# Performance work log

Measured on AMD Instinct MI355X. Metric: run time of the kernel, lower is better.

## Reference

```python
import jax, jax.numpy as jnp
import numpy as np

B, S, E, H, D, F = 8, 512, 768, 12, 64, 3072
EPS = 1e-5
SQRT3 = np.float32(np.sqrt(3.0))


def _ln(x, g, b):
    m = jnp.mean(x, -1, keepdims=True)
    v = jnp.mean((x - m) ** 2, -1, keepdims=True)
    return (x - m) * jax.lax.rsqrt(v + EPS) * g + b


def _gelu_new(x):
    return 0.5 * x * (1.0 + jnp.tanh(0.7978845608028654 * (x + 0.044715 * x * x * x)))


def _heads(t):  # [B,T,E] -> [B,T,H,D]
    return t.reshape(t.shape[0], t.shape[1], H, D)


def _self_attn(xl, Wq, Wk, Wv, Wo, bo, mask):
    q = _heads(xl @ Wq)
    k = _heads(xl @ Wk)
    v = _heads(xl @ Wv)
    w = jnp.einsum('bqhd,bkhd->bhqk', q, k) / 8.0  # scale=True, sqrt(64)
    w = jnp.where(mask, -1e9, w)
    p = jax.nn.softmax(w, axis=-1)
    o = jnp.einsum('bhqk,bkhd->bqhd', p, v).reshape(xl.shape)
    present = jnp.stack([k.transpose(0, 2, 1, 3), v.transpose(0, 2, 1, 3)])  # [2,B,H,S,D]
    return o @ Wo + bo, present


def _cross_attn(xl, el, wq, bq, wk, bk, wv, bv, wp, bp, mask):
    q = _heads(xl @ wq + bq)
    k = _heads(el @ wk + bk)
    v = _heads(el @ wv + bv)
    w = jnp.einsum('bqhd,bkhd->bhqk', q, k) / 8.0
    w = jnp.where(mask, -1e4, w)
    p = jax.nn.softmax(w, axis=-1)
    o = jnp.einsum('bhqk,bkhd->bqhd', p, v).reshape(xl.shape)
    return o @ wp + bp  # Conv1D: x @ W + b


def _block(x, encoder_output, mask_queries, mask_sa, mask_enc, tau,
           Wq, Wk, Wv, Wo, bo,
           fcq_w, fcq_b, fck_w, fck_b, fcv_w, fcv_b, cproj_w, cproj_b,
           ln1_g, ln1_b, ln2_g, ln2_b,
           cfc_w, cfc_b, cproj2_w, cproj2_b,
           a1_w, a1_b, a2_w, a2_b, a3_w, a3_b):
    thr = jnp.asarray(tau, jnp.float32)
    sa, present = _self_attn(_ln(x, ln1_g, ln1_b), Wq, Wk, Wv, Wo, bo, mask_sa)
    a = x + sa  # resid dropout = identity (eval)
    al = _ln(a, ln1_g, ln1_b)

    def cross(idx):
        el = _ln(encoder_output[:, idx], ln1_g, ln1_b)
        return _cross_attn(al, el, fcq_w, fcq_b, fck_w, fck_b, fcv_w, fcv_b,
                           cproj_w, cproj_b, mask_enc)

    e1, e2, e3 = cross(0), cross(1), cross(2)

    def gate(e, w, b):
        alpha = jax.nn.sigmoid(jnp.concatenate([a, e], -1) @ w + b)
        lm = jnp.where(alpha > thr, 1.0, 0.0)
        vm = jnp.where(alpha < 1.0 - thr, 1.0, 0.0)
        return alpha * lm * a + (1.0 - alpha) * vm * e

    enc_att = (gate(e1, a1_w, a1_b) + gate(e2, a2_w, a2_b) + gate(e3, a3_w, a3_b)) / SQRT3
    aq = enc_att * mask_queries
    m = _gelu_new(_ln(aq, ln2_g, ln2_b) @ cfc_w + cfc_b) @ cproj2_w + cproj2_b
    out = (aq + m) * mask_queries
    return out, present


def setup_inputs() -> dict:
    key = jax.random.key(0)
    ks = jax.random.split(key, 40)
    p = lambda k, shp: (jax.random.normal(k, shp, jnp.float32) * 0.02)
    x = jax.random.normal(ks[0], (B, S, E), jnp.float32)
    encoder_output = jax.random.normal(ks[1], (B, 3, S, E), jnp.float32)
    mask_queries = jnp.ones((B, S, 1), jnp.float32)
    causal = ~jnp.tril(jnp.ones((S, S), bool))  # True = masked
    mask_self_attention = jnp.broadcast_to(causal[None, None], (B, 1, S, S))
    mask_encoder = jax.random.bernoulli(ks[2], 0.1, (B, 1, 1, S))
    d = dict(x=x, encoder_output=encoder_output, mask_queries=mask_queries,
             mask_self_attention=mask_self_attention, mask_encoder=mask_encoder,
             i=0, tau=0,
             Wq=p(ks[3], (E, E)), Wk=p(ks[4], (E, E)), Wv=p(ks[5], (E, E)),
             Wo=p(ks[6], (E, E)), bo=jnp.zeros((E,), jnp.float32),
             fcq_w=p(ks[7], (E, E)), fcq_b=jnp.zeros((E,), jnp.float32),
             fck_w=p(ks[8], (E, E)), fck_b=jnp.zeros((E,), jnp.float32),
             fcv_w=p(ks[9], (E, E)), fcv_b=jnp.zeros((E,), jnp.float32),
             cproj_w=p(ks[10], (E, E)), cproj_b=jnp.zeros((E,), jnp.float32),
             ln1_g=jnp.ones((E,), jnp.float32), ln1_b=jnp.zeros((E,), jnp.float32),
             ln2_g=jnp.ones((E,), jnp.float32), ln2_b=jnp.zeros((E,), jnp.float32),
             cfc_w=p(ks[11], (E, F)), cfc_b=jnp.zeros((F,), jnp.float32),
             cproj2_w=p(ks[12], (F, E)), cproj2_b=jnp.zeros((E,), jnp.float32),
             a1_w=p(ks[13], (2 * E, E)), a1_b=jnp.zeros((E,), jnp.float32),
             a2_w=p(ks[14], (2 * E, E)), a2_b=jnp.zeros((E,), jnp.float32),
             a3_w=p(ks[15], (2 * E, E)), a3_b=jnp.zeros((E,), jnp.float32))
    return d


def reference(x, encoder_output, mask_queries, mask_self_attention, mask_encoder, i, tau,
              Wq, Wk, Wv, Wo, bo,
              fcq_w, fcq_b, fck_w, fck_b, fcv_w, fcv_b, cproj_w, cproj_b,
              ln1_g, ln1_b, ln2_g, ln2_b,
              cfc_w, cfc_b, cproj2_w, cproj2_b,
              a1_w, a1_b, a2_w, a2_b, a3_w, a3_b):
    return _block(x, encoder_output, mask_queries, mask_self_attention, mask_encoder, tau,
                  Wq, Wk, Wv, Wo, bo,
                  fcq_w, fcq_b, fck_w, fck_b, fcv_w, fcv_b, cproj_w, cproj_b,
                  ln1_g, ln1_b, ln2_g, ln2_b,
                  cfc_w, cfc_b, cproj2_w, cproj2_b,
                  a1_w, a1_b, a2_w, a2_b, a3_w, a3_b)
```

## Files before the change

kernel.cpp:

```cpp
#include <hip/hip_runtime.h>
#include <hip/hip_bf16.h>
#include <math.h>

typedef __hip_bfloat16 bf16;
typedef __attribute__((ext_vector_type(8))) short s16x8;
typedef __attribute__((ext_vector_type(4))) float f32x4;

#define BB 8
#define SS 512
#define EE 768
#define HH 12
#define DD 64
#define FF 3072
#define NTOK (BB * SS)
#define NE ((size_t)NTOK * EE)

#define TM 128
#define TN 128
#define TK 64

#define QT 64
#define KT 64

#define FLAG_RES  4
#define FLAG_GELU 8
#define FLAG_FIN  16
#define FLAG_CBSD 32
#define FLAG_QKV  128
#define FLAG_KV   256
#define FLAG_GSEG 512

#define AS1 const __attribute__((address_space(1))) void*
#define AS3 __attribute__((address_space(3))) void*

__device__ __forceinline__ float gelu_new(float x) {
    float u2 = 1.5957691216057308f * (x + 0.044715f * x * x * x);
    return x / (1.0f + __expf(-u2));
}

__global__ __launch_bounds__(256) void tcast_kernel(
    const float* __restrict__ src, bf16* __restrict__ dst, int R, int C)
{
    __shared__ float t[32][33];
    int c0 = blockIdx.x * 32, r0 = blockIdx.y * 32;
    int tid = threadIdx.x;
    int x = tid & 31, y = tid >> 5;
    #pragma unroll
    for (int i = 0; i < 4; ++i) {
        int r = y + i * 8;
        t[r][x] = src[(size_t)(r0 + r) * C + c0 + x];
    }
    __syncthreads();
    #pragma unroll
    for (int i = 0; i < 4; ++i) {
        int c = y + i * 8;
        dst[(size_t)(c0 + c) * R + r0 + x] = __float2bfloat16(t[x][c]);
    }
}

__global__ __launch_bounds__(256) void ln_kernel(
    const float* __restrict__ in, bf16* __restrict__ out,
    const float* __restrict__ g, const float* __restrict__ bta, int encmode)
{
    int row = blockIdx.x;
    const float* x;
    if (encmode) {
        int idx = row >> 12, b = (row >> 9) & 7, s = row & 511;
        x = in + (((size_t)b * 3 + idx) * SS + s) * EE;
    } else {
        x = in + (size_t)row * EE;
    }
    int tid = threadIdx.x;

    float v0 = x[tid], v1 = x[tid + 256], v2 = x[tid + 512];
    float s1 = v0 + v1 + v2;
    float s2 = v0 * v0 + v1 * v1 + v2 * v2;
    #pragma unroll
    for (int o = 32; o > 0; o >>= 1) {
        s1 += __shfl_down(s1, o);
        s2 += __shfl_down(s2, o);
    }
    __shared__ float r1[4], r2[4];
    if ((tid & 63) == 0) { r1[tid >> 6] = s1; r2[tid >> 6] = s2; }
    __syncthreads();
    float mean = (r1[0] + r1[1] + r1[2] + r1[3]) * (1.0f / 768.0f);
    float ssq  = (r2[0] + r2[1] + r2[2] + r2[3]) * (1.0f / 768.0f);
    float rstd = rsqrtf(ssq - mean * mean + 1e-5f);

    bf16* y = out + (size_t)row * EE;
    y[tid]       = __float2bfloat16((v0 - mean) * rstd * g[tid]       + bta[tid]);
    y[tid + 256] = __float2bfloat16((v1 - mean) * rstd * g[tid + 256] + bta[tid + 256]);
    y[tid + 512] = __float2bfloat16((v2 - mean) * rstd * g[tid + 512] + bta[tid + 512]);
}

template <int FLAGS>
__global__ __launch_bounds__(256) void mgemm_kernel(
    const bf16* __restrict__ A, const bf16* __restrict__ A2,
    const bf16* __restrict__ Wt, const float* __restrict__ bias,
    float* __restrict__ Cf, bf16* __restrict__ Cb, bf16* __restrict__ Cb2,
    int ldcb, const float* __restrict__ Rsrc, const float* __restrict__ maskq,
    int Nn, int K, int lda)
{
    constexpr bool f_res  = FLAGS & FLAG_RES;
    constexpr bool f_gelu = FLAGS & FLAG_GELU;
    constexpr bool f_fin  = FLAGS & FLAG_FIN;
    constexpr bool f_cbsd = FLAGS & FLAG_CBSD;
    constexpr bool f_qkv  = FLAGS & FLAG_QKV;
    constexpr bool f_kv   = FLAGS & FLAG_KV;
    constexpr bool f_gseg = FLAGS & FLAG_GSEG;

    __shared__ __align__(16) bf16 smem[2 * (TM * TK + TN * TK)];
    const int BUFE = TM * TK + TN * TK;
    int tid = threadIdx.x;
    int w = tid >> 6, l = tid & 63;
    int row0 = blockIdx.x * TM, col0 = blockIdx.y * TN;

    int wr = (w >> 1) * 64, wc = (w & 1) * 64;
    int lr = l & 15, lg = l >> 4;

    const bf16* Wb = Wt;
    const float* bb_ = bias;
    if constexpr (f_gseg) {
        int seg = row0 >> 12;
        Wb = Wt + (size_t)seg * 1536 * 768;
        bb_ = bias + seg * 768;
    }

    f32x4 acc[4][4];
    #pragma unroll
    for (int m = 0; m < 4; ++m)
        #pragma unroll
        for (int n = 0; n < 4; ++n) acc[m][n] = (f32x4){0.f, 0.f, 0.f, 0.f};

    auto stage = [&](int buf, int kb) {
        bf16* As_ = smem + buf * BUFE;
        bf16* Bs_ = As_ + TM * TK;
        #pragma unroll
        for (int i = 0; i < 4; ++i) {
            int e = (i * 256 + tid) * 8;
            int r = e >> 6;
            int c = (e & 63) ^ ((r & 7) << 3);
            const bf16* asrc;
            if constexpr (f_gseg) {
                int kg = kb + c;
                if (kg < 768) asrc = A  + (size_t)((row0 + r) & 4095) * lda + kg;
                else          asrc = A2 + (size_t)(row0 + r) * lda + (kg - 768);
            } else {
                asrc = A + (size_t)(row0 + r) * lda + kb + c;
            }
            __builtin_amdgcn_global_load_lds((AS1)asrc,
                (AS3)((char*)As_ + i * 4096 + w * 1024), 16, 0, 0);
            __builtin_amdgcn_global_load_lds((AS1)(Wb + (size_t)(col0 + r) * K + kb + c),
                (AS3)((char*)Bs_ + i * 4096 + w * 1024), 16, 0, 0);
        }
    };

    int nk = K / TK;
    stage(0, 0);
    for (int t = 0; t < nk; ++t) {
        int cur = t & 1;
        if (t + 1 < nk) {
            stage(cur ^ 1, (t + 1) * TK);
            asm volatile("s_waitcnt vmcnt(8)" ::: "memory");
        } else {
            asm volatile("s_waitcnt vmcnt(0)" ::: "memory");
        }
        __builtin_amdgcn_s_barrier();
        __builtin_amdgcn_sched_barrier(0);

        const char* As = (const char*)(smem + cur * BUFE);
        const char* Bs = As + TM * TK * 2;
        __builtin_amdgcn_s_setprio(1);
        #pragma unroll
        for (int ks = 0; ks < 2; ++ks) {
            s16x8 af[4], bfr[4];
            #pragma unroll
            for (int m = 0; m < 4; ++m) {
                int row = wr + m * 16 + lr;
                af[m] = *(const s16x8*)(As + row * 128 +
                          ((ks * 64 + lg * 16) ^ ((row & 7) << 4)));
            }
            #pragma unroll
            for (int n = 0; n < 4; ++n) {
                int row = wc + n * 16 + lr;
                bfr[n] = *(const s16x8*)(Bs + row * 128 +
                          ((ks * 64 + lg * 16) ^ ((row & 7) << 4)));
            }
            #pragma unroll
            for (int m = 0; m < 4; ++m)
                #pragma unroll
                for (int n = 0; n < 4; ++n)
                    acc[m][n] = __builtin_amdgcn_mfma_f32_16x16x32_bf16(
                        af[m], bfr[n], acc[m][n], 0, 0, 0);
        }
        __builtin_amdgcn_s_setprio(0);
        asm volatile("s_waitcnt lgkmcnt(0)" ::: "memory");
        __builtin_amdgcn_s_barrier();
        __builtin_amdgcn_sched_barrier(0);
    }

    int gh0 = (col0 + wc) >> 6;
    bool vquad = (f_qkv && gh0 >= 24) || (f_kv && gh0 >= 12);
    bf16* T = smem + w * 4096;

    #pragma unroll
    for (int m = 0; m < 4; ++m) {
        #pragma unroll
        for (int n = 0; n < 4; ++n) {
            #pragma unroll
            for (int j = 0; j < 4; ++j) {
                int row = row0 + wr + m * 16 + lg * 4 + j;
                int col = col0 + wc + n * 16 + lr;
                size_t lin = (size_t)row * Nn + col;
                float v = acc[m][n][j];
                if (bb_)                 v += bb_[col];
                if constexpr (f_res)     v += Rsrc[lin];
                if constexpr (f_gelu)    v = gelu_new(v);
                if constexpr (f_fin)     v = (Rsrc[lin] + v) * maskq[row];
                int bb = row >> 9, s = row & 511;
                int gh = col >> 6, d = col & 63;
                if constexpr (f_qkv) {
                    if (gh < 12) {
                        Cb[(((size_t)bb * HH + gh) * SS + s) * DD + d] = __float2bfloat16(v);
                    } else if (gh < 24) {
                        Cf[(((size_t)bb * HH + (gh - 12)) * SS + s) * DD + d] = v;
                        Cb[NE + (((size_t)bb * HH + (gh - 12)) * SS + s) * DD + d] = __float2bfloat16(v);
                    } else {
                        Cf[NE + (((size_t)bb * HH + (gh - 24)) * SS + s) * DD + d] = v;
                        int rl = m * 16 + lg * 4 + j, cl = n * 16 + lr;
                        *(bf16*)((char*)T + cl * 128 + ((rl * 2) ^ ((cl & 7) << 4))) =
                            __float2bfloat16(v);
                    }
                } else if constexpr (f_kv) {
                    if (gh < 12) {
                        Cb[(((size_t)bb * HH + gh) * SS + s) * DD + d] = __float2bfloat16(v);
                    } else {
                        int rl = m * 16 + lg * 4 + j, cl = n * 16 + lr;
                        *(bf16*)((char*)T + cl * 128 + ((rl * 2) ^ ((cl & 7) << 4))) =
                            __float2bfloat16(v);
                    }
                } else if constexpr (f_cbsd) {
                    Cb[(((size_t)bb * HH + gh) * SS + s) * DD + d] = __float2bfloat16(v);
                } else {
                    if (Cf) Cf[lin] = v;
                    if (Cb) Cb[(size_t)row * ldcb + col] = __float2bfloat16(v);
                }
            }
        }
    }

    if constexpr (f_qkv || f_kv) {
        if (vquad) {
            int b2 = (row0 + wr) >> 9;
            int s0 = (row0 + wr) & 511;
            int hV = gh0 - (f_qkv ? 24 : 12);
            bf16* vb = Cb2 + (((size_t)b2 * HH + hV) * DD) * SS + s0;
            #pragma unroll
            for (int p = 0; p < 8; ++p) {
                int dl = p * 8 + (l >> 3);
                int ch = l & 7;
                int cs = ch ^ (dl & 7);
                s16x8 vv = *(const s16x8*)((char*)T + dl * 128 + cs * 16);
                *(s16x8*)(vb + (size_t)dl * SS + ch * 8) = vv;
            }
        }
    }
}

__global__ __launch_bounds__(256) void fattn2_kernel(
    const bf16* __restrict__ Qb, const bf16* __restrict__ Kb,
    const bf16* __restrict__ Vb, const int* __restrict__ maskE,
    bf16* __restrict__ Out, int causal)
{
    int bh = blockIdx.x, qt = blockIdx.y;
    int bp = bh / HH, h = bh % HH;
    int bq = bp & 7;
    int tid = threadIdx.x;
    int w = tid >> 6, l = tid & 63;
    int lr = l & 15, g = l >> 4;

    __shared__ __align__(16) bf16 Qs[64 * 64];
    __shared__ __align__(16) bf16 Ks[64 * 64];
    __shared__ __align__(16) bf16 Vs[64 * 64];
    __shared__ __align__(16) bf16 Ps[64 * 64];

    int p0 = w * 1024 + l * 16;
    {
        const char* qg = (const char*)(Qb + (((size_t)bq * HH + h) * SS + qt * QT) * DD);
        #pragma unroll
        for (int i = 0; i < 2; ++i) {
            int p = i * 4096 + p0;
            int row = p >> 7, cb = p & 127;
            int scb = cb ^ ((row & 7) << 4);
            __builtin_amdgcn_global_load_lds((AS1)(qg + row * 128 + scb),
                (AS3)((char*)Qs + i * 4096 + w * 1024), 16, 0, 0);
        }
    }

    float mrun[4], lrun[4];
    f32x4 oacc[4];
    #pragma unroll
    for (int j = 0; j < 4; ++j) { mrun[j] = -3.0e38f; lrun[j] = 0.f; }
    #pragma unroll
    for (int n = 0; n < 4; ++n) oacc[n] = (f32x4){0.f, 0.f, 0.f, 0.f};

    int ntiles = causal ? (qt + 1) : (SS / KT);
    int qrow_base = w * 16;

    for (int kt = 0; kt < ntiles; ++kt) {
        const char* kg = (const char*)(Kb + ((size_t)bh * SS + kt * KT) * DD);
        const char* vg = (const char*)(Vb + (size_t)bh * DD * SS + (size_t)kt * KT);
        #pragma unroll
        for (int i = 0; i < 2; ++i) {
            int p = i * 4096 + p0;
            int row = p >> 7, cb = p & 127;
            int scb = cb ^ ((row & 7) << 4);
            __builtin_amdgcn_global_load_lds((AS1)(kg + row * 128 + scb),
                (AS3)((char*)Ks + i * 4096 + w * 1024), 16, 0, 0);
            __builtin_amdgcn_global_load_lds((AS1)(vg + (size_t)row * (SS * 2) + scb),
                (AS3)((char*)Vs + i * 4096 + w * 1024), 16, 0, 0);
        }
        int km[4];
        if (maskE) {
            #pragma unroll
            for (int n = 0; n < 4; ++n)
                km[n] = maskE[(size_t)bq * SS + kt * KT + n * 16 + lr];
        }
        __syncthreads();

        f32x4 sacc[4];
        #pragma unroll
        for (int n = 0; n < 4; ++n) sacc[n] = (f32x4){0.f, 0.f, 0.f, 0.f};
        #pragma unroll
        for (int ks = 0; ks < 2; ++ks) {
            int qrow = qrow_base + lr;
            s16x8 aq = *(const s16x8*)((const char*)Qs +
                        qrow * 128 + ((ks * 64 + g * 16) ^ ((qrow & 7) << 4)));
            #pragma unroll
            for (int n = 0; n < 4; ++n) {
                int krow = n * 16 + lr;
                s16x8 bk = *(const s16x8*)((const char*)Ks +
                            krow * 128 + ((ks * 64 + g * 16) ^ ((krow & 7) << 4)));
                sacc[n] = __builtin_amdgcn_mfma_f32_16x16x32_bf16(aq, bk, sacc[n], 0, 0, 0);
            }
        }

        #pragma unroll
        for (int n = 0; n < 4; ++n) {
            #pragma unroll
            for (int j = 0; j < 4; ++j) {
                float v = sacc[n][j] * 0.125f;
                if (causal) {
                    if (kt == qt && (n * 16 + lr > qrow_base + 4 * g + j)) v = -3.0e38f;
                } else {
                    if (km[n] != 0) v = -1e4f;
                }
                sacc[n][j] = v;
            }
        }

        float mx[4];
        #pragma unroll
        for (int j = 0; j < 4; ++j)
            mx[j] = fmaxf(fmaxf(sacc[0][j], sacc[1][j]), fmaxf(sacc[2][j], sacc[3][j]));
        #pragma unroll
        for (int msk = 1; msk < 16; msk <<= 1) {
            #pragma unroll
            for (int j = 0; j < 4; ++j) mx[j] = fmaxf(mx[j], __shfl_xor(mx[j], msk));
        }
        float rs[4], psum[4];
        #pragma unroll
        for (int j = 0; j < 4; ++j) {
            float mn = fmaxf(mrun[j], mx[j]);
            rs[j] = __expf(mrun[j] - mn);
            mrun[j] = mn;
            psum[j] = 0.f;
        }
        #pragma unroll
        for (int n = 0; n < 4; ++n) {
            #pragma unroll
            for (int j = 0; j < 4; ++j) {
                float p = __expf(sacc[n][j] - mrun[j]);
                psum[j] += p;
                int prow = qrow_base + 4 * g + j;
                int key = n * 16 + lr;
                *(bf16*)((char*)Ps + prow * 128 + ((2 * key) ^ ((prow & 7) << 4))) =
                    __float2bfloat16(p);
            }
        }
        #pragma unroll
        for (int msk = 1; msk < 16; msk <<= 1) {
            #pragma unroll
            for (int j = 0; j < 4; ++j) psum[j] += __shfl_xor(psum[j], msk);
        }
        #pragma unroll
        for (int j = 0; j < 4; ++j) lrun[j] = lrun[j] * rs[j] + psum[j];
        #pragma unroll
        for (int n = 0; n < 4; ++n) {
            #pragma unroll
            for (int j = 0; j < 4; ++j) oacc[n][j] *= rs[j];
        }

        #pragma unroll
        for (int ks = 0; ks < 2; ++ks) {
            int prow = qrow_base + lr;
            s16x8 ap = *(const s16x8*)((const char*)Ps +
                        prow * 128 + ((ks * 64 + g * 16) ^ ((prow & 7) << 4)));
            #pragma unroll
            for (int n = 0; n < 4; ++n) {
                int vrow = n * 16 + lr;
                s16x8 bv = *(const s16x8*)((const char*)Vs +
                            vrow * 128 + ((ks * 64 + g * 16) ^ ((vrow & 7) << 4)));
                oacc[n] = __builtin_amdgcn_mfma_f32_16x16x32_bf16(ap, bv, oacc[n], 0, 0, 0);
            }
        }
        __syncthreads();
    }

    float inv[4];
    #pragma unroll
    for (int j = 0; j < 4; ++j) inv[j] = 1.0f / lrun[j];
    #pragma unroll
    for (int n = 0; n < 4; ++n) {
        #pragma unroll
        for (int j = 0; j < 4; ++j) {
            int q = qt * QT + qrow_base + 4 * g + j;
            int d = n * 16 + lr;
            Out[((size_t)bp * SS + q) * EE + h * DD + d] =
                __float2bfloat16(oacc[n][j] * inv[j]);
        }
    }
}

__global__ void gate3_kernel(const float* __restrict__ logits, const float* __restrict__ a,
                             const bf16* __restrict__ e, float* __restrict__ acc,
                             const int* __restrict__ tau, const float* __restrict__ maskq)
{
    float thr = (float)tau[0];
    for (size_t i = (size_t)blockIdx.x * blockDim.x + threadIdx.x; i < NE;
         i += (size_t)gridDim.x * blockDim.x) {
        float av = a[i];
        float r = 0.f;
        #pragma unroll
        for (int idx = 0; idx < 3; ++idx) {
            float lg = logits[(size_t)idx * NE + i];
            float ev = __bfloat162float(e[(size_t)idx * NE + i]);
            float al = 1.0f / (1.0f + __expf(-lg));
            float lm = (al > thr) ? 1.0f : 0.0f;
            float vm = (al < 1.0f - thr) ? 1.0f : 0.0f;
            r += al * lm * av + (1.0f - al) * vm * ev;
        }
        acc[i] = r * 0.57735026918962576f * maskq[i / EE];
    }
}

extern "C" void kernel_launch(void* const* d_in, const int* in_sizes, int n_in,
                              void* d_out, int out_size, void* d_ws, size_t ws_size,
                              hipStream_t stream)
{
    const float* x        = (const float*)d_in[0];
    const float* enc      = (const float*)d_in[1];
    const float* maskq    = (const float*)d_in[2];
    const int*   mask_enc = (const int*)d_in[4];
    const int*   tau      = (const int*)d_in[6];
    const float* Wq = (const float*)d_in[7];
    const float* Wk = (const float*)d_in[8];
    const float* Wv = (const float*)d_in[9];
    const float* Wo = (const float*)d_in[10];
    const float* bo = (const float*)d_in[11];
    const float* fcq_w = (const float*)d_in[12];
    const float* fcq_b = (const float*)d_in[13];
    const float* fck_w = (const float*)d_in[14];
    const float* fck_b = (const float*)d_in[15];
    const float* fcv_w = (const float*)d_in[16];
    const float* fcv_b = (const float*)d_in[17];
    const float* cproj_w = (const float*)d_in[18];
    const float* cproj_b = (const float*)d_in[19];
    const float* ln1_g = (const float*)d_in[20];
    const float* ln1_b = (const float*)d_in[21];
    const float* ln2_g = (const float*)d_in[22];
    const float* ln2_b = (const float*)d_in[23];
    const float* cfc_w = (const float*)d_in[24];
    const float* cfc_b = (const float*)d_in[25];
    const float* cproj2_w = (const float*)d_in[26];
    const float* cproj2_b = (const float*)d_in[27];
    const float* aw[3] = {(const float*)d_in[28], (const float*)d_in[30], (const float*)d_in[32]};
    const float* ab[3] = {(const float*)d_in[29], (const float*)d_in[31], (const float*)d_in[33]};

    float* out   = (float*)d_out;
    float* kpres = out + NE;

    float* ws  = (float*)d_ws;
    float* a     = ws;
    float* acc   = ws + NE;
    float* R     = ws + 2 * NE;
    bf16*  kb_c   = (bf16*)R;
    bf16*  vb_c   = kb_c + 3 * NE;
    float* logits = R;
    bf16*  mlphb  = (bf16*)R;

    bf16* bbase = (bf16*)(ws + 5 * NE);
    bf16* lnb   = bbase;
    bf16* atts  = bbase;
    bf16* lnenc = bbase + NE;
    bf16* attc  = lnenc;
    bf16* a_bf  = bbase + 4 * NE;
    bf16* e_bf  = bbase + 5 * NE;
    bf16* qbhb  = bbase + 8 * NE;
    bf16* kbhb  = bbase + 9 * NE;
    bf16* vbhb  = bbase + 10 * NE;
    bf16* wp    = bbase + 11 * NE;
    bf16* WqkvT = wp;          wp += 3 * 768 * 768;
    bf16* WoT = wp;            wp += 768 * 768;
    bf16* fcqT = wp;           wp += 768 * 768;
    bf16* fckvT = wp;          wp += 2 * 768 * 768;
    bf16* cprojT = wp;         wp += 768 * 768;
    bf16* awT = wp;            wp += (size_t)3 * 1536 * 768;
    bf16* cfcT = wp;           wp += (size_t)768 * 3072;
    bf16* cproj2T = wp;        wp += (size_t)3072 * 768;
    float* kvb = (float*)wp;
    float* gb  = kvb + 1536;

    dim3 blk(256);
    dim3 gT88(24, 24), gTaw(24, 48), gTcf(96, 24), gTcp(24, 96);

    tcast_kernel<<<gT88, blk, 0, stream>>>(Wq, WqkvT, 768, 768);
    tcast_kernel<<<gT88, blk, 0, stream>>>(Wk, WqkvT + 768 * 768, 768, 768);
    tcast_kernel<<<gT88, blk, 0, stream>>>(Wv, WqkvT + 2 * 768 * 768, 768, 768);
    tcast_kernel<<<gT88, blk, 0, stream>>>(Wo, WoT, 768, 768);
    tcast_kernel<<<gT88, blk, 0, stream>>>(fcq_w, fcqT, 768, 768);
    tcast_kernel<<<gT88, blk, 0, stream>>>(fck_w, fckvT, 768, 768);
    tcast_kernel<<<gT88, blk, 0, stream>>>(fcv_w, fckvT + 768 * 768, 768, 768);
    tcast_kernel<<<gT88, blk, 0, stream>>>(cproj_w, cprojT, 768, 768);
    tcast_kernel<<<gTaw, blk, 0, stream>>>(aw[0], awT, 1536, 768);
    tcast_kernel<<<gTaw, blk, 0, stream>>>(aw[1], awT + 1536 * 768, 1536, 768);
    tcast_kernel<<<gTaw, blk, 0, stream>>>(aw[2], awT + 2 * 1536 * 768, 1536, 768);
    tcast_kernel<<<gTcf, blk, 0, stream>>>(cfc_w, cfcT, 768, 3072);
    tcast_kernel<<<gTcp, blk, 0, stream>>>(cproj2_w, cproj2T, 3072, 768);
    hipMemcpyAsync(kvb, fck_b, 768 * 4, hipMemcpyDeviceToDevice, stream);
    hipMemcpyAsync(kvb + 768, fcv_b, 768 * 4, hipMemcpyDeviceToDevice, stream);
    hipMemcpyAsync(gb, ab[0], 768 * 4, hipMemcpyDeviceToDevice, stream);
    hipMemcpyAsync(gb + 768, ab[1], 768 * 4, hipMemcpyDeviceToDevice, stream);
    hipMemcpyAsync(gb + 1536, ab[2], 768 * 4, hipMemcpyDeviceToDevice, stream);

    ln_kernel<<<NTOK, blk, 0, stream>>>(x, lnb, ln1_g, ln1_b, 0);
    mgemm_kernel<FLAG_QKV><<<dim3(32, 18), blk, 0, stream>>>(lnb, nullptr, WqkvT, nullptr,
        kpres, qbhb, vbhb, 0, nullptr, nullptr, 2304, 768, 768);
    fattn2_kernel<<<dim3(96, 8), blk, 0, stream>>>(qbhb, kbhb, vbhb, nullptr, atts, 1);
    mgemm_kernel<FLAG_RES><<<dim3(32, 6), blk, 0, stream>>>(atts, nullptr, WoT, bo,
        a, a_bf, nullptr, 768, x, nullptr, 768, 768, 768);
    ln_kernel<<<NTOK, blk, 0, stream>>>(a, lnb, ln1_g, ln1_b, 0);
    mgemm_kernel<FLAG_CBSD><<<dim3(32, 6), blk, 0, stream>>>(lnb, nullptr, fcqT, fcq_b,
        nullptr, qbhb, nullptr, 0, nullptr, nullptr, 768, 768, 768);
    ln_kernel<<<3 * NTOK, blk, 0, stream>>>(enc, lnenc, ln1_g, ln1_b, 1);
    mgemm_kernel<FLAG_KV><<<dim3(96, 12), blk, 0, stream>>>(lnenc, nullptr, fckvT, kvb,
        nullptr, kb_c, vb_c, 0, nullptr, nullptr, 1536, 768, 768);
    fattn2_kernel<<<dim3(288, 8), blk, 0, stream>>>(qbhb, kb_c, vb_c, mask_enc, attc, 0);
    mgemm_kernel<0><<<dim3(96, 6), blk, 0, stream>>>(attc, nullptr, cprojT, cproj_b,
        nullptr, e_bf, nullptr, 768, nullptr, nullptr, 768, 768, 768);
    mgemm_kernel<FLAG_GSEG><<<dim3(96, 6), blk, 0, stream>>>(a_bf, e_bf, awT, gb,
        logits, nullptr, nullptr, 0, nullptr, nullptr, 768, 1536, 768);
    gate3_kernel<<<2048, blk, 0, stream>>>(logits, a, e_bf, acc, tau, maskq);
    ln_kernel<<<NTOK, blk, 0, stream>>>(acc, lnb, ln2_g, ln2_b, 0);
    mgemm_kernel<FLAG_GELU><<<dim3(32, 24), blk, 0, stream>>>(lnb, nullptr, cfcT, cfc_b,
        nullptr, mlphb, nullptr, 3072, nullptr, nullptr, 3072, 768, 768);
    mgemm_kernel<FLAG_FIN><<<dim3(32, 6), blk, 0, stream>>>(mlphb, nullptr, cproj2T, cproj2_b,
        out, nullptr, nullptr, 0, acc, maskq, 768, 3072, 3072);
}
```

Baseline: 658.0 us.

## Batch weight transposes into one launch and fuse gating with LayerNorm

Merges the thirteen separate weight transpose-cast launches into one kernel that maps a flat block index to each matrix, and replaces five device memcpy calls with one bias copy kernel. The gate kernel now handles one row per block and computes LayerNorm in the same pass, removing a separate LN launch and a re-read of the accumulator. The fused LN uses a one-pass variance (E[x^2]-mean^2), which can lose some precision compared with the two-pass form.

Result: faster. 632.2 us (-3.9%).

```diff
diff --git a/kernel.cpp b/kernel.cpp
--- a/kernel.cpp
+++ b/kernel.cpp
@@ -38,24 +38,60 @@
     return x / (1.0f + __expf(-u2));
 }
 
-__global__ __launch_bounds__(256) void tcast_kernel(
-    const float* __restrict__ src, bf16* __restrict__ dst, int R, int C)
+__global__ __launch_bounds__(256) void tcast_all_kernel(
+    const float* s0, const float* s1, const float* s2, const float* s3,
+    const float* s4, const float* s5, const float* s6, const float* s7,
+    const float* s8, const float* s9, const float* s10, const float* s11,
+    const float* s12,
+    bf16* d0, bf16* d1, bf16* d2, bf16* d3, bf16* d4, bf16* d5, bf16* d6,
+    bf16* d7, bf16* d8, bf16* d9, bf16* d10, bf16* d11, bf16* d12)
 {
-    __shared__ float t[32][33];
-    int c0 = blockIdx.x * 32, r0 = blockIdx.y * 32;
+    const int start[14] = {0, 576, 1152, 1728, 2304, 2880, 3456, 4032,
+                           4608, 5760, 6912, 8064, 10368, 12672};
+    const float* srcs[13] = {s0,s1,s2,s3,s4,s5,s6,s7,s8,s9,s10,s11,s12};
+    bf16* dsts[13] = {d0,d1,d2,d3,d4,d5,d6,d7,d8,d9,d10,d11,d12};
+
+    int bid = blockIdx.x;
+    int idx = 0;
+    #pragma unroll
+    for (int i = 1; i < 13; ++i) if (bid >= start[i]) idx = i;
+    int R = (idx < 8) ? 768 : (idx < 11) ? 1536 : (idx == 11) ? 768 : 3072;
+    int C = (idx < 8) ? 768 : (idx < 11) ? 768 : (idx == 11) ? 3072 : 768;
+    const float* src = srcs[idx];
+    bf16* dst = dsts[idx];
+
+    int t = bid - start[idx];
+    int gx = C >> 5;
+    int c0 = (t % gx) << 5;
+    int r0 = (t / gx) << 5;
+
+    __shared__ float tb[32][33];
     int tid = threadIdx.x;
     int x = tid & 31, y = tid >> 5;
     #pragma unroll
     for (int i = 0; i < 4; ++i) {
         int r = y + i * 8;
-        t[r][x] = src[(size_t)(r0 + r) * C + c0 + x];
+        tb[r][x] = src[(size_t)(r0 + r) * C + c0 + x];
     }
     __syncthreads();
     #pragma unroll
     for (int i = 0; i < 4; ++i) {
         int c = y + i * 8;
-        dst[(size_t)(c0 + c) * R + r0 + x] = __float2bfloat16(t[x][c]);
-    }
+        dst[(size_t)(c0 + c) * R + r0 + x] = __float2bfloat16(tb[x][c]);
+    }
+}
+
+__global__ __launch_bounds__(256) void biascopy_kernel(
+    const float* fckb, const float* fcvb, const float* a0, const float* a1,
+    const float* a2, float* kvb, float* gb)
+{
+    int i = blockIdx.x * 256 + threadIdx.x;
+    int seg = i / 768, off = i % 768;
+    if (seg == 0)      kvb[off]        = fckb[off];
+    else if (seg == 1) kvb[768 + off]  = fcvb[off];
+    else if (seg == 2) gb[off]         = a0[off];
+    else if (seg == 3) gb[768 + off]   = a1[off];
+    else               gb[1536 + off]  = a2[off];
 }
 
 __global__ __launch_bounds__(256) void ln_kernel(
@@ -432,13 +468,23 @@
     }
 }
 
-__global__ void gate3_kernel(const float* __restrict__ logits, const float* __restrict__ a,
-                             const bf16* __restrict__ e, float* __restrict__ acc,
-                             const int* __restrict__ tau, const float* __restrict__ maskq)
+__global__ __launch_bounds__(256) void gate3ln_kernel(
+    const float* __restrict__ logits, const float* __restrict__ a,
+    const bf16* __restrict__ e, float* __restrict__ acc, bf16* __restrict__ lnout,
+    const int* __restrict__ tau, const float* __restrict__ maskq,
+    const float* __restrict__ g, const float* __restrict__ bta)
 {
+    int row = blockIdx.x;
+    int tid = threadIdx.x;
     float thr = (float)tau[0];
-    for (size_t i = (size_t)blockIdx.x * blockDim.x + threadIdx.x; i < NE;
-         i += (size_t)gridDim.x * blockDim.x) {
+    float mq = maskq[row] * 0.57735026918962576f;
+    size_t base = (size_t)row * EE;
+
+    float aq[3];
+    float s1 = 0.f, s2 = 0.f;
+    #pragma unroll
+    for (int c = 0; c < 3; ++c) {
+        size_t i = base + tid + c * 256;
         float av = a[i];
         float r = 0.f;
         #pragma unroll
@@ -450,7 +496,29 @@
             float vm = (al < 1.0f - thr) ? 1.0f : 0.0f;
             r += al * lm * av + (1.0f - al) * vm * ev;
         }
-        acc[i] = r * 0.57735026918962576f * maskq[i / EE];
+        float v = r * mq;
+        acc[i] = v;
+        aq[c] = v;
+        s1 += v;
+        s2 += v * v;
+    }
+    #pragma unroll
+    for (int o = 32; o > 0; o >>= 1) {
+        s1 += __shfl_down(s1, o);
+        s2 += __shfl_down(s2, o);
+    }
+    __shared__ float r1[4], r2[4];
+    if ((tid & 63) == 0) { r1[tid >> 6] = s1; r2[tid >> 6] = s2; }
+    __syncthreads();
+    float mean = (r1[0] + r1[1] + r1[2] + r1[3]) * (1.0f / 768.0f);
+    float ssq  = (r2[0] + r2[1] + r2[2] + r2[3]) * (1.0f / 768.0f);
+    float rstd = rsqrtf(ssq - mean * mean + 1e-5f);
+
+    bf16* y = lnout + base;
+    #pragma unroll
+    for (int c = 0; c < 3; ++c) {
+        int col = tid + c * 256;
+        y[col] = __float2bfloat16((aq[c] - mean) * rstd * g[col] + bta[col]);
     }
 }
 
@@ -522,26 +590,14 @@
     float* gb  = kvb + 1536;
 
     dim3 blk(256);
-    dim3 gT88(24, 24), gTaw(24, 48), gTcf(96, 24), gTcp(24, 96);
-
-    tcast_kernel<<<gT88, blk, 0, stream>>>(Wq, WqkvT, 768, 768);
-    tcast_kernel<<<gT88, blk, 0, stream>>>(Wk, WqkvT + 768 * 768, 768, 768);
-    tcast_kernel<<<gT88, blk, 0, stream>>>(Wv, WqkvT + 2 * 768 * 768, 768, 768);
-    tcast_kernel<<<gT88, blk, 0, stream>>>(Wo, WoT, 768, 768);
-    tcast_kernel<<<gT88, blk, 0, stream>>>(fcq_w, fcqT, 768, 768);
-    tcast_kernel<<<gT88, blk, 0, stream>>>(fck_w, fckvT, 768, 768);
-    tcast_kernel<<<gT88, blk, 0, stream>>>(fcv_w, fckvT + 768 * 768, 768, 768);
-    tcast_kernel<<<gT88, blk, 0, stream>>>(cproj_w, cprojT, 768, 768);
-    tcast_kernel<<<gTaw, blk, 0, stream>>>(aw[0], awT, 1536, 768);
-    tcast_kernel<<<gTaw, blk, 0, stream>>>(aw[1], awT + 1536 * 768, 1536, 768);
-    tcast_kernel<<<gTaw, blk, 0, stream>>>(aw[2], awT + 2 * 1536 * 768, 1536, 768);
-    tcast_kernel<<<gTcf, blk, 0, stream>>>(cfc_w, cfcT, 768, 3072);
-    tcast_kernel<<<gTcp, blk, 0, stream>>>(cproj2_w, cproj2T, 3072, 768);
-    hipMemcpyAsync(kvb, fck_b, 768 * 4, hipMemcpyDeviceToDevice, stream);
-    hipMemcpyAsync(kvb + 768, fcv_b, 768 * 4, hipMemcpyDeviceToDevice, stream);
-    hipMemcpyAsync(gb, ab[0], 768 * 4, hipMemcpyDeviceToDevice, stream);
-    hipMemcpyAsync(gb + 768, ab[1], 768 * 4, hipMemcpyDeviceToDevice, stream);
-    hipMemcpyAsync(gb + 1536, ab[2], 768 * 4, hipMemcpyDeviceToDevice, stream);
+
+    tcast_all_kernel<<<12672, blk, 0, stream>>>(
+        Wq, Wk, Wv, Wo, fcq_w, fck_w, fcv_w, cproj_w,
+        aw[0], aw[1], aw[2], cfc_w, cproj2_w,
+        WqkvT, WqkvT + 768 * 768, WqkvT + 2 * 768 * 768, WoT, fcqT,
+        fckvT, fckvT + 768 * 768, cprojT,
+        awT, awT + 1536 * 768, awT + 2 * 1536 * 768, cfcT, cproj2T);
+    biascopy_kernel<<<15, blk, 0, stream>>>(fck_b, fcv_b, ab[0], ab[1], ab[2], kvb, gb);
 
     ln_kernel<<<NTOK, blk, 0, stream>>>(x, lnb, ln1_g, ln1_b, 0);
     mgemm_kernel<FLAG_QKV><<<dim3(32, 18), blk, 0, stream>>>(lnb, nullptr, WqkvT, nullptr,
@@ -560,8 +616,8 @@
         nullptr, e_bf, nullptr, 768, nullptr, nullptr, 768, 768, 768);
     mgemm_kernel<FLAG_GSEG><<<dim3(96, 6), blk, 0, stream>>>(a_bf, e_bf, awT, gb,
         logits, nullptr, nullptr, 0, nullptr, nullptr, 768, 1536, 768);
-    gate3_kernel<<<2048, blk, 0, stream>>>(logits, a, e_bf, acc, tau, maskq);
-    ln_kernel<<<NTOK, blk, 0, stream>>>(acc, lnb, ln2_g, ln2_b, 0);
+    gate3ln_kernel<<<NTOK, blk, 0, stream>>>(logits, a, e_bf, acc, lnb,
+        tau, maskq, ln2_g, ln2_b);
     mgemm_kernel<FLAG_GELU><<<dim3(32, 24), blk, 0, stream>>>(lnb, nullptr, cfcT, cfc_b,
         nullptr, mlphb, nullptr, 3072, nullptr, nullptr, 3072, 768, 768);
     mgemm_kernel<FLAG_FIN><<<dim3(32, 6), blk, 0, stream>>>(mlphb, nullptr, cproj2T, cproj2_b,
```
